# Optimization experiments

Hardware: AMD Instinct MI355X
Metric: run time of the kernel (lower is better)

## Reference

```python
import jax, jax.numpy as jnp
import numpy as np
import math

B, T, C = 2, 1400, 256
H = 16
D = C // H            # 16
FF = 1024
VOCAB = 1400
SLOTS = 256
EPS = 1e-5


def _ln(x, g, b):
    m = jnp.mean(x, axis=-1, keepdims=True)
    v = jnp.mean(jnp.square(x - m), axis=-1, keepdims=True)
    return (x - m) * jax.lax.rsqrt(v + EPS) * g + b


def setup_inputs() -> dict:
    key = jax.random.key(0)
    ks = jax.random.split(key, 24)
    s = 0.02
    inp = {
        "x": jax.random.normal(ks[0], (B, T, C), dtype=jnp.float32),
        "disease_ids": jax.random.randint(ks[1], (B, T), 0, VOCAB),
        # nn.MultiheadAttention params (torch layout: [out,in])
        "in_proj_w": jax.random.normal(ks[2], (3 * C, C)) * s,
        "in_proj_b": jnp.zeros((3 * C,), jnp.float32),
        "out_proj_w": jax.random.normal(ks[3], (C, C)) * s,
        "out_proj_b": jnp.zeros((C,), jnp.float32),
        # LayerNorms
        "ln1_g": jnp.ones((C,), jnp.float32), "ln1_b": jnp.zeros((C,), jnp.float32),
        "ln2_g": jnp.ones((C,), jnp.float32), "ln2_b": jnp.zeros((C,), jnp.float32),
        "ln3_g": jnp.ones((C,), jnp.float32), "ln3_b": jnp.zeros((C,), jnp.float32),
        # DiseaseGraphAttention
        "gq_w": jax.random.normal(ks[4], (C, C)) * s, "gq_b": jnp.zeros((C,), jnp.float32),
        "gk_w": jax.random.normal(ks[5], (C, C)) * s, "gk_b": jnp.zeros((C,), jnp.float32),
        "gv_w": jax.random.normal(ks[6], (C, C)) * s, "gv_b": jnp.zeros((C,), jnp.float32),
        "go_w": jax.random.normal(ks[7], (C, C)) * s, "go_b": jnp.zeros((C,), jnp.float32),
        "affinity": jax.random.normal(ks[8], (VOCAB, VOCAB)) * 0.01,
        # LongTermMemoryBank (only the read path affects the returned output)
        "mem_bank": jax.random.normal(ks[9], (SLOTS, C)) * 0.1,
        "read_w": jax.random.normal(ks[10], (SLOTS, C)) * s,
        "read_b": jnp.zeros((SLOTS,), jnp.float32),
        # FFN
        "ffn_w1": jax.random.normal(ks[11], (FF, C)) * s, "ffn_b1": jnp.zeros((FF,), jnp.float32),
        "ffn_w2": jax.random.normal(ks[12], (C, FF)) * s, "ffn_b2": jnp.zeros((C,), jnp.float32),
    }
    return inp


def reference(x, disease_ids, in_proj_w, in_proj_b, out_proj_w, out_proj_b,
              ln1_g, ln1_b, ln2_g, ln2_b, ln3_g, ln3_b,
              gq_w, gq_b, gk_w, gk_b, gv_w, gv_b, go_w, go_b, affinity,
              mem_bank, read_w, read_b, ffn_w1, ffn_b1, ffn_w2, ffn_b2):
    scale = 1.0 / math.sqrt(D)

    # ---- standard MHA (pre-norm, residual), dropout in eval mode ----
    h = _ln(x, ln1_g, ln1_b)
    qkv = h @ in_proj_w.T + in_proj_b                      # [B,T,3C]
    q, k, v = jnp.split(qkv, 3, axis=-1)
    q = q.reshape(B, T, H, D); k = k.reshape(B, T, H, D); v = v.reshape(B, T, H, D)
    scores = jnp.einsum('bthd,bshd->bhts', q, k) * scale   # [B,H,T,T]
    attn = jax.nn.softmax(scores, axis=-1)
    o = jnp.einsum('bhts,bshd->bthd', attn, v).reshape(B, T, C)
    x = x + (o @ out_proj_w.T + out_proj_b)

    # ---- disease-graph attention with gathered affinity bias ----
    h = _ln(x, ln2_g, ln2_b)
    q = (h @ gq_w.T + gq_b).reshape(B, T, H, D)
    k = (h @ gk_w.T + gk_b).reshape(B, T, H, D)
    v = (h @ gv_w.T + gv_b).reshape(B, T, H, D)
    aff = affinity[disease_ids]                            # [B,T,VOCAB] (VOCAB == T)
    scores = jnp.einsum('bthd,bshd->bhts', q, k) * scale + aff[:, None, :, :] * 0.1
    attn = jax.nn.softmax(scores, axis=-1)
    o = jnp.einsum('bhts,bshd->bthd', attn, v).reshape(B, T, C)
    x = x + (o @ go_w.T + go_b)

    # ---- memory-bank read (write/erase only mutate params, not the output) ----
    read_weights = jax.nn.softmax(x @ read_w.T + read_b, axis=-1)   # [B,T,SLOTS]
    x = x + jnp.einsum('bts,sc->btc', read_weights, mem_bank)

    # ---- FFN ----
    h = _ln(x, ln3_g, ln3_b)
    ff = jax.nn.gelu(h @ ffn_w1.T + ffn_b1, approximate=False) @ ffn_w2.T + ffn_b2
    return x + ff
```

## Files before the change

### kernel.cpp

```cpp
#include <hip/hip_runtime.h>
#include <hip/hip_bf16.h>
#include <math.h>

namespace {

typedef __attribute__((ext_vector_type(4))) float f32x4;
typedef __attribute__((ext_vector_type(8))) short s16x8;
typedef __attribute__((ext_vector_type(4))) short s16x4;
typedef unsigned short ushort_t;

constexpr int kB = 2, kT = 1400, kC = 256, kH = 16, kFF = 1024;
constexpr int kBT = kB * kT;
constexpr float kEps = 1e-5f;
constexpr int kSP = 5;
constexpr int kSLen = 280;
constexpr int SBLK = 288;
constexpr int KPITCH = 24;
constexpr float kQScale   = 0.25f * 1.4426950408889634f;
constexpr float kAffScale = 0.1f * 1.4426950408889634f;

__device__ __forceinline__ ushort_t f2bf(float f) {
    unsigned u = __float_as_uint(f);
    u += 0x7fffu + ((u >> 16) & 1u);
    return (ushort_t)(u >> 16);
}
__device__ __forceinline__ float bf2f(ushort_t u) {
    return __uint_as_float(((unsigned)u) << 16);
}
__device__ __forceinline__ unsigned pk2bf(float a, float b) {
    __hip_bfloat162 t = __float22bfloat162_rn(make_float2(a, b));
    union { __hip_bfloat162 h; unsigned u; } cv; cv.h = t;
    return cv.u;
}
__device__ __forceinline__ float fast_exp2(float x) {
    float r;
    asm("v_exp_f32 %0, %1" : "=v"(r) : "v"(x));
    return r;
}

__global__ __launch_bounds__(256) void convert_kernel(
        const float* __restrict__ in_proj_w, const float* __restrict__ gq_w,
        const float* __restrict__ gk_w, const float* __restrict__ gv_w,
        const float* __restrict__ out_proj_w, const float* __restrict__ go_w,
        const float* __restrict__ ffn_w1, const float* __restrict__ ffn_w2,
        const float* __restrict__ read_w, const float* __restrict__ mem_bank,
        const float* __restrict__ gq_b, const float* __restrict__ gk_b,
        const float* __restrict__ gv_b,
        ushort_t* __restrict__ wdst, float* __restrict__ gqkvb) {
    const int bid = blockIdx.x, tid = threadIdx.x;
    if (bid == 608) {
        gqkvb[tid] = gq_b[tid];
        gqkvb[256 + tid] = gk_b[tid];
        gqkvb[512 + tid] = gv_b[tid];
        return;
    }
    const int u0 = (bid * 256 + tid) * 8;
    if (u0 >= 1114112) {
        #pragma unroll
        for (int j = 0; j < 8; j++) {
            const int d = u0 - 1114112 + j;
            wdst[1114112 + d] = f2bf(mem_bank[(d & 255) * 256 + (d >> 8)]);
        }
        return;
    }
    const float* src; int off;
    if      (u0 < 196608)  { src = in_proj_w;  off = u0; }
    else if (u0 < 262144)  { src = gq_w;       off = u0 - 196608; }
    else if (u0 < 327680)  { src = gk_w;       off = u0 - 262144; }
    else if (u0 < 393216)  { src = gv_w;       off = u0 - 327680; }
    else if (u0 < 458752)  { src = out_proj_w; off = u0 - 393216; }
    else if (u0 < 524288)  { src = go_w;       off = u0 - 458752; }
    else if (u0 < 786432)  { src = ffn_w1;     off = u0 - 524288; }
    else if (u0 < 1048576) { src = ffn_w2;     off = u0 - 786432; }
    else                   { src = read_w;     off = u0 - 1048576; }
    #pragma unroll
    for (int j = 0; j < 8; j++) wdst[u0 + j] = f2bf(src[off + j]);
}

__global__ __launch_bounds__(256) void qkvln_kernel(
        const float* __restrict__ xin, const ushort_t* __restrict__ hin,
        const float* __restrict__ lng, const float* __restrict__ lnb,
        const ushort_t* __restrict__ W, const float* __restrict__ bias,
        ushort_t* __restrict__ outQ, ushort_t* __restrict__ outK,
        ushort_t* __restrict__ outV) {
    __shared__ ushort_t dsA[16 * 256];
    const int tid = threadIdx.x;
    const int lane = tid & 63, wave = tid >> 6;
    const int qi = lane & 15, g = lane >> 4;
    const int m0 = blockIdx.x * 16;

    if (xin) {
        const int r = tid >> 4, e = tid & 15;
        const float* xr = xin + (size_t)(m0 + r) * 256 + e * 16;
        const float4 v0 = *(const float4*)&xr[0];
        const float4 v1 = *(const float4*)&xr[4];
        const float4 v2 = *(const float4*)&xr[8];
        const float4 v3 = *(const float4*)&xr[12];
        float s1 = ((v0.x + v0.y) + (v0.z + v0.w)) + ((v1.x + v1.y) + (v1.z + v1.w))
                 + ((v2.x + v2.y) + (v2.z + v2.w)) + ((v3.x + v3.y) + (v3.z + v3.w));
        float s2 = ((v0.x * v0.x + v0.y * v0.y) + (v0.z * v0.z + v0.w * v0.w))
                 + ((v1.x * v1.x + v1.y * v1.y) + (v1.z * v1.z + v1.w * v1.w))
                 + ((v2.x * v2.x + v2.y * v2.y) + (v2.z * v2.z + v2.w * v2.w))
                 + ((v3.x * v3.x + v3.y * v3.y) + (v3.z * v3.z + v3.w * v3.w));
        s1 += __shfl_xor(s1, 1); s2 += __shfl_xor(s2, 1);
        s1 += __shfl_xor(s1, 2); s2 += __shfl_xor(s2, 2);
        s1 += __shfl_xor(s1, 4); s2 += __shfl_xor(s2, 4);
        s1 += __shfl_xor(s1, 8); s2 += __shfl_xor(s2, 8);
        const float mean = s1 * (1.f / 256.f);
        const float rstd = rsqrtf(s2 * (1.f / 256.f) - mean * mean + kEps);
        const int c0 = e * 16;
        const float4 ga = *(const float4*)&lng[c0];
        const float4 gb = *(const float4*)&lng[c0 + 4];
        const float4 gc = *(const float4*)&lng[c0 + 8];
        const float4 gd = *(const float4*)&lng[c0 + 12];
        const float4 ba = *(const float4*)&lnb[c0];
        const float4 bb = *(const float4*)&lnb[c0 + 4];
        const float4 bc = *(const float4*)&lnb[c0 + 8];
        const float4 bd = *(const float4*)&lnb[c0 + 12];
        union { unsigned u4[4]; s16x8 s; } p0, p1;
        p0.u4[0] = pk2bf((v0.x - mean) * rstd * ga.x + ba.x,
                         (v0.y - mean) * rstd * ga.y + ba.y);
        p0.u4[1] = pk2bf((v0.z - mean) * rstd * ga.z + ba.z,
                         (v0.w - mean) * rstd * ga.w + ba.w);
        p0.u4[2] = pk2bf((v1.x - mean) * rstd * gb.x + bb.x,
                         (v1.y - mean) * rstd * gb.y + bb.y);
        p0.u4[3] = pk2bf((v1.z - mean) * rstd * gb.z + bb.z,
                         (v1.w - mean) * rstd * gb.w + bb.w);
        p1.u4[0] = pk2bf((v2.x - mean) * rstd * gc.x + bc.x,
                         (v2.y - mean) * rstd * gc.y + bc.y);
        p1.u4[1] = pk2bf((v2.z - mean) * rstd * gc.z + bc.z,
                         (v2.w - mean) * rstd * gc.w + bc.w);
        p1.u4[2] = pk2bf((v3.x - mean) * rstd * gd.x + bd.x,
                         (v3.y - mean) * rstd * gd.y + bd.y);
        p1.u4[3] = pk2bf((v3.z - mean) * rstd * gd.z + bd.z,
                         (v3.w - mean) * rstd * gd.w + bd.w);
        const int cg0 = e * 2, cg1 = e * 2 + 1;
        *(s16x8*)&dsA[r * 256 + ((cg0 ^ (r & 7)) << 3)] = p0.s;
        *(s16x8*)&dsA[r * 256 + ((cg1 ^ (r & 7)) << 3)] = p1.s;
    } else {
        const int r = tid >> 4, e = tid & 15;
        const ushort_t* hr = hin + (size_t)(m0 + r) * 256 + e * 16;
        #pragma unroll
        for (int i = 0; i < 2; i++) {
            const s16x8 v = *(const s16x8*)&hr[i * 8];
            const int cg = e * 2 + i;
            *(s16x8*)&dsA[r * 256 + ((cg ^ (r & 7)) << 3)] = v;
        }
    }
    __syncthreads();
    f32x4 acc[12] = {};
    const int cbase = wave * 192;
    for (int kt = 0; kt < 8; ++kt) {
        const int cg = kt * 4 + g;
        const s16x8 af = *(const s16x8*)&dsA[qi * 256 + ((cg ^ (qi & 7)) << 3)];
        #pragma unroll
        for (int nn = 0; nn < 12; ++nn) {
            const int wr = cbase + nn * 16 + qi;
            const s16x8 bf = *(const s16x8*)&W[(size_t)wr * 256 + kt * 32 + g * 8];
            acc[nn] = __builtin_amdgcn_mfma_f32_16x16x32_bf16(af, bf, acc[nn], 0, 0, 0);
        }
    }
    #pragma unroll
    for (int nn = 0; nn < 12; ++nn) {
        const int col = cbase + nn * 16 + qi;
        const float bv = bias[col];
        const int hh = (col & 255) >> 4, dd = col & 15;
        #pragma unroll
        for (int r = 0; r < 4; ++r) {
            const int gm = m0 + 4 * g + r;
            const int b = (gm >= kT) ? 1 : 0;
            const int ss = gm - b * kT;
            const size_t hoff = (((size_t)(b * 16 + hh)) * kT + ss) * 16 + dd;
            const float v = acc[nn][r] + bv;
            if (col < 256)      outQ[hoff] = f2bf(v * kQScale);
            else if (col < 512) outK[hoff] = f2bf(v);
            else                outV[hoff] = f2bf(v);
        }
    }
}

__global__ __launch_bounds__(256) void ffn_kernel(
        const ushort_t* __restrict__ hin, const ushort_t* __restrict__ wF1,
        const float* __restrict__ b1, const ushort_t* __restrict__ wF2,
        const float* __restrict__ b2, const float* __restrict__ x3,
        float* __restrict__ out) {
    __shared__ ushort_t dsH[16 * 256];
    __shared__ ushort_t dsF[16 * 1024];
    const int tid = threadIdx.x;
    const int lane = tid & 63, wave = tid >> 6;
    const int qi = lane & 15, g = lane >> 4;
    const int wn = wave * 64;
    const int m0 = blockIdx.x * 16;

    {
        const int r = tid >> 4, e = tid & 15;
        const ushort_t* hr = hin + (size_t)(m0 + r) * 256 + e * 16;
        #pragma unroll
        for (int i = 0; i < 2; i++) {
            const s16x8 v = *(const s16x8*)&hr[i * 8];
            const int cg = e * 2 + i;
            *(s16x8*)&dsH[r * 256 + ((cg ^ (r & 7)) << 3)] = v;
        }
    }
    __syncthreads();
    #pragma unroll
    for (int cc = 0; cc < 4; ++cc) {
        f32x4 acc[4] = {};
        for (int kt = 0; kt < 8; ++kt) {
            const int cg = kt * 4 + g;
            const s16x8 af = *(const s16x8*)&dsH[qi * 256 + ((cg ^ (qi & 7)) << 3)];
            #pragma unroll
            for (int nn = 0; nn < 4; ++nn) {
                const int wr = cc * 256 + wn + nn * 16 + qi;
                const s16x8 bf = *(const s16x8*)&wF1[(size_t)wr * 256 + kt * 32 + g * 8];
                acc[nn] = __builtin_amdgcn_mfma_f32_16x16x32_bf16(af, bf, acc[nn], 0, 0, 0);
            }
        }
        #pragma unroll
        for (int nn = 0; nn < 4; ++nn) {
            const int col = cc * 256 + wn + nn * 16 + qi;
            const float bv = b1[col];
            #pragma unroll
            for (int r = 0; r < 4; ++r) {
                const int row = 4 * g + r;
                float v = acc[nn][r] + bv;
                v = 0.5f * v * (1.f + erff(v * 0.70710678f));
                const int cg = col >> 3, e = col & 7;
                dsF[row * 1024 + ((cg ^ (row & 7)) << 3) + e] = f2bf(v);
            }
        }
    }
    __syncthreads();
    f32x4 acc2[4] = {};
    for (int kt = 0; kt < 32; ++kt) {
        const int cg = kt * 4 + g;
        const s16x8 af = *(const s16x8*)&dsF[qi * 1024 + ((cg ^ (qi & 7)) << 3)];
        #pragma unroll
        for (int nn = 0; nn < 4; ++nn) {
            const int wr = wn + nn * 16 + qi;
            const s16x8 bf = *(const s16x8*)&wF2[(size_t)wr * 1024 + kt * 32 + g * 8];
            acc2[nn] = __builtin_amdgcn_mfma_f32_16x16x32_bf16(af, bf, acc2[nn], 0, 0, 0);
        }
    }
    #pragma unroll
    for (int nn = 0; nn < 4; ++nn) {
        const int col = wn + nn * 16 + qi;
        const float bv = b2[col];
        #pragma unroll
        for (int r = 0; r < 4; ++r) {
            const int row = 4 * g + r;
            const size_t idx = (size_t)(m0 + row) * 256 + col;
            out[idx] = acc2[nn][r] + bv + x3[idx];
        }
    }
}

__global__ __launch_bounds__(256) void gemmcomb_kernel(
        const ushort_t* __restrict__ o_part, const float* __restrict__ l_part,
        const ushort_t* __restrict__ W, const float* __restrict__ bias,
        const float* __restrict__ res,
        const float* __restrict__ lng, const float* __restrict__ lnb,
        float* __restrict__ outf, ushort_t* __restrict__ outln) {
    __shared__ ushort_t dsA[16 * 256];
    __shared__ float ws1[4][16], ws2[4][16];
    const int tid = threadIdx.x;
    const int lane = tid & 63, wave = tid >> 6;
    const int qi = lane & 15, g = lane >> 4;
    const int wn = wave * 64;
    const int m0 = blockIdx.x * 16;

    {
        const int h = tid >> 4, r = tid & 15;
        const int gm = m0 + r;
        const int b = (gm >= kT) ? 1 : 0;
        const int t = gm - b * kT;
        float f[16] = {};
        float l = 0.f;
        #pragma unroll
        for (int p = 0; p < kSP; ++p) {
            const size_t sl_ = (size_t)((b * kSP + p) * 16 + h);
            l += l_part[sl_ * kT + t];
            const s16x8 v0 = *(const s16x8*)&o_part[(sl_ * kT + t) * 16];
            const s16x8 v1 = *(const s16x8*)&o_part[(sl_ * kT + t) * 16 + 8];
            #pragma unroll
            for (int j = 0; j < 8; j++) {
                f[j]     += bf2f((ushort_t)v0[j]);
                f[8 + j] += bf2f((ushort_t)v1[j]);
            }
        }
        const float li = 1.f / l;
        union { unsigned u4[4]; s16x8 s; } p0, p1;
        p0.u4[0] = pk2bf(f[0] * li, f[1] * li);
        p0.u4[1] = pk2bf(f[2] * li, f[3] * li);
        p0.u4[2] = pk2bf(f[4] * li, f[5] * li);
        p0.u4[3] = pk2bf(f[6] * li, f[7] * li);
        p1.u4[0] = pk2bf(f[8] * li, f[9] * li);
        p1.u4[1] = pk2bf(f[10] * li, f[11] * li);
        p1.u4[2] = pk2bf(f[12] * li, f[13] * li);
        p1.u4[3] = pk2bf(f[14] * li, f[15] * li);
        const int cg0 = h * 2, cg1 = h * 2 + 1;
        *(s16x8*)&dsA[r * 256 + ((cg0 ^ (r & 7)) << 3)] = p0.s;
        *(s16x8*)&dsA[r * 256 + ((cg1 ^ (r & 7)) << 3)] = p1.s;
    }
    __syncthreads();
    f32x4 acc[4] = {};
    for (int kt = 0; kt < 8; ++kt) {
        const int cg = kt * 4 + g;
        const s16x8 af = *(const s16x8*)&dsA[qi * 256 + ((cg ^ (qi & 7)) << 3)];
        #pragma unroll
        for (int nn = 0; nn < 4; ++nn) {
            const int wr = wn + nn * 16 + qi;
            const s16x8 bf = *(const s16x8*)&W[(size_t)wr * 256 + kt * 32 + g * 8];
            acc[nn] = __builtin_amdgcn_mfma_f32_16x16x32_bf16(af, bf, acc[nn], 0, 0, 0);
        }
    }
    float v[4][4];
    float s1[4] = {0.f, 0.f, 0.f, 0.f}, s2[4] = {0.f, 0.f, 0.f, 0.f};
    #pragma unroll
    for (int nn = 0; nn < 4; ++nn) {
        #pragma unroll
        for (int r = 0; r < 4; ++r) {
            const int row = 4 * g + r, col = wn + nn * 16 + qi;
            const size_t idx = (size_t)(m0 + row) * 256 + col;
            const float t = acc[nn][r] + bias[col] + res[idx];
            outf[idx] = t;
            v[nn][r] = t;
            s1[r] += t; s2[r] += t * t;
        }
    }
    if (outln) {
        #pragma unroll
        for (int r = 0; r < 4; ++r) {
            s1[r] += __shfl_xor(s1[r], 1); s2[r] += __shfl_xor(s2[r], 1);
            s1[r] += __shfl_xor(s1[r], 2); s2[r] += __shfl_xor(s2[r], 2);
            s1[r] += __shfl_xor(s1[r], 4); s2[r] += __shfl_xor(s2[r], 4);
            s1[r] += __shfl_xor(s1[r], 8); s2[r] += __shfl_xor(s2[r], 8);
        }
        if (qi == 0) {
            #pragma unroll
            for (int r = 0; r < 4; ++r) { ws1[wave][4 * g + r] = s1[r]; ws2[wave][4 * g + r] = s2[r]; }
        }
        __syncthreads();
        #pragma unroll
        for (int r = 0; r < 4; ++r) {
            const int row = 4 * g + r;
            const float S1 = ws1[0][row] + ws1[1][row] + ws1[2][row] + ws1[3][row];
            const float S2 = ws2[0][row] + ws2[1][row] + ws2[2][row] + ws2[3][row];
            const float mean = S1 * (1.f / 256.f);
            const float rstd = rsqrtf(S2 * (1.f / 256.f) - mean * mean + kEps);
            #pragma unroll
            for (int nn = 0; nn < 4; ++nn) {
                const int col = wn + nn * 16 + qi;
                outln[(size_t)(m0 + row) * 256 + col] =
                    f2bf((v[nn][r] - mean) * rstd * lng[col] + lnb[col]);
            }
        }
    }
}

__global__ __launch_bounds__(256) void memread_kernel(
        const float* __restrict__ x2, const ushort_t* __restrict__ wRead,
        const float* __restrict__ read_b, const ushort_t* __restrict__ wMemT,
        const float* __restrict__ lng, const float* __restrict__ lnb,
        float* __restrict__ xout, ushort_t* __restrict__ outln) {
    __shared__ ushort_t dsP[16 * 256];
    __shared__ float lsum[4][16];
    __shared__ float lt[16];
    __shared__ float ws1[4][16], ws2[4][16];
    const int tid = threadIdx.x;
    const int lane = tid & 63, wave = tid >> 6;
    const int qi = lane & 15, g = lane >> 4;
    const int wn = wave * 64;
    const int m0 = blockIdx.x * 16;

    {
        const int r = tid >> 4, e = tid & 15;
        const float* xr = x2 + (size_t)(m0 + r) * 256 + e * 16;
        #pragma unroll
        for (int i = 0; i < 2; i++) {
            const float4 va = *(const float4*)&xr[i * 8];
            const float4 vb = *(const float4*)&xr[i * 8 + 4];
            union { unsigned u4[4]; s16x8 s; } pu;
            pu.u4[0] = pk2bf(va.x, va.y);
            pu.u4[1] = pk2bf(va.z, va.w);
            pu.u4[2] = pk2bf(vb.x, vb.y);
            pu.u4[3] = pk2bf(vb.z, vb.w);
            const int cg = e * 2 + i;
            *(s16x8*)&dsP[r * 256 + ((cg ^ (r & 7)) << 3)] = pu.s;
        }
    }
    __syncthreads();
    f32x4 acc[4] = {};
    for (int kt = 0; kt < 8; ++kt) {
        const int cg = kt * 4 + g;
        const s16x8 af = *(const s16x8*)&dsP[qi * 256 + ((cg ^ (qi & 7)) << 3)];
        #pragma unroll
        for (int nn = 0; nn < 4; ++nn) {
            const int wr = wn + nn * 16 + qi;
            const s16x8 bf = *(const s16x8*)&wRead[(size_t)wr * 256 + kt * 32 + g * 8];
            acc[nn] = __builtin_amdgcn_mfma_f32_16x16x32_bf16(af, bf, acc[nn], 0, 0, 0);
        }
    }
    float p[4][4];
    float rs[4] = {0.f, 0.f, 0.f, 0.f};
    #pragma unroll
    for (int nn = 0; nn < 4; ++nn) {
        const float bb = read_b[wn + nn * 16 + qi];
        #pragma unroll
        for (int r = 0; r < 4; ++r) {
            p[nn][r] = __expf(acc[nn][r] + bb);
            rs[r] += p[nn][r];
        }
    }
    #pragma unroll
    for (int r = 0; r < 4; ++r) {
        rs[r] += __shfl_xor(rs[r], 1);
        rs[r] += __shfl_xor(rs[r], 2);
        rs[r] += __shfl_xor(rs[r], 4);
        rs[r] += __shfl_xor(rs[r], 8);
    }
    __syncthreads();
    if (qi == 0) {
        #pragma unroll
        for (int r = 0; r < 4; ++r) lsum[wave][4 * g + r] = rs[r];
    }
    #pragma unroll
    for (int nn = 0; nn < 4; ++nn) {
        #pragma unroll
        for (int r = 0; r < 4; ++r) {
            const int row = 4 * g + r, col = wn + nn * 16 + qi;
            const int cg = col >> 3, e = col & 7;
            dsP[row * 256 + ((cg ^ (row & 7)) << 3) + e] = f2bf(p[nn][r]);
        }
    }
    __syncthreads();
    if (tid < 16)
        lt[tid] = 1.f / (lsum[0][tid] + lsum[1][tid] + lsum[2][tid] + lsum[3][tid]);
    __syncthreads();
    f32x4 acc2[4] = {};
    for (int kt = 0; kt < 8; ++kt) {
        const int cg = kt * 4 + g;
        const s16x8 af = *(const s16x8*)&dsP[qi * 256 + ((cg ^ (qi & 7)) << 3)];
        #pragma unroll
        for (int nn = 0; nn < 4; ++nn) {
            const int wr = wn + nn * 16 + qi;
            const s16x8 bf = *(const s16x8*)&wMemT[(size_t)wr * 256 + kt * 32 + g * 8];
            acc2[nn] = __builtin_amdgcn_mfma_f32_16x16x32_bf16(af, bf, acc2[nn], 0, 0, 0);
        }
    }
    float xo[4][4];
    float s1[4] = {0.f, 0.f, 0.f, 0.f}, s2[4] = {0.f, 0.f, 0.f, 0.f};
    #pragma unroll
    for (int nn = 0; nn < 4; ++nn) {
        #pragma unroll
        for (int r = 0; r < 4; ++r) {
            const int row = 4 * g + r;
            const size_t idx = (size_t)(m0 + row) * 256 + wn + nn * 16 + qi;
            const float t = acc2[nn][r] * lt[row] + x2[idx];
            xout[idx] = t;
            xo[nn][r] = t;
            s1[r] += t; s2[r] += t * t;
        }
    }
    #pragma unroll
    for (int r = 0; r < 4; ++r) {
        s1[r] += __shfl_xor(s1[r], 1); s2[r] += __shfl_xor(s2[r], 1);
        s1[r] += __shfl_xor(s1[r], 2); s2[r] += __shfl_xor(s2[r], 2);
        s1[r] += __shfl_xor(s1[r], 4); s2[r] += __shfl_xor(s2[r], 4);
        s1[r] += __shfl_xor(s1[r], 8); s2[r] += __shfl_xor(s2[r], 8);
    }
    if (qi == 0) {
        #pragma unroll
        for (int r = 0; r < 4; ++r) { ws1[wave][4 * g + r] = s1[r]; ws2[wave][4 * g + r] = s2[r]; }
    }
    __syncthreads();
    #pragma unroll
    for (int r = 0; r < 4; ++r) {
        const int row = 4 * g + r;
        const float S1 = ws1[0][row] + ws1[1][row] + ws1[2][row] + ws1[3][row];
        const float S2 = ws2[0][row] + ws2[1][row] + ws2[2][row] + ws2[3][row];
        const float mean = S1 * (1.f / 256.f);
        const float rstd = rsqrtf(S2 * (1.f / 256.f) - mean * mean + kEps);
        #pragma unroll
        for (int nn = 0; nn < 4; ++nn) {
            const int col = wn + nn * 16 + qi;
            outln[(size_t)(m0 + row) * 256 + col] =
                f2bf((xo[nn][r] - mean) * rstd * lng[col] + lnb[col]);
        }
    }
}

template <bool kAff>
__global__ __launch_bounds__(512) void attn_mfma_kernel(
        const ushort_t* __restrict__ q, const ushort_t* __restrict__ kbuf,
        const ushort_t* __restrict__ vbuf, ushort_t* __restrict__ o_part,
        float* __restrict__ l_part,
        const float* __restrict__ affinity, const int* __restrict__ did) {
    __shared__ ushort_t ldsK[SBLK * KPITCH];
    __shared__ ushort_t ldsV[SBLK * 16];
    const int tid  = threadIdx.x;
    const int bid  = blockIdx.x;
    const int w    = (bid & 7) * 220 + (bid >> 3);
    const int slice = w / 11;
    const int ttile = w - slice * 11;
    const int h    = slice & 15;
    const int z    = slice >> 4;
    const int b    = (z >= 5) ? 1 : 0;
    const int sp   = z - b * 5;
    const int t0   = ttile * 128;
    const int s0   = sp * kSLen;
    const int lane = tid & 63;
    const int wave = tid >> 6;
    const int g    = lane >> 4;
    const int qi   = lane & 15;

    const int tq  = t0 + wave * 16 + qi;
    const int tqc = min(tq, kT - 1);
    const ushort_t* qhb = q + (size_t)(b * 16 + h) * kT * 16;
    s16x8 qb = {0, 0, 0, 0, 0, 0, 0, 0};
    if (g < 2) qb = *(const s16x8*)&qhb[(size_t)tqc * 16 + g * 8];
    const float* ar = nullptr;
    if (kAff) ar = affinity + (size_t)did[b * kT + tqc] * kT;

    const ushort_t* kb  = kbuf + (size_t)(b * 16 + h) * kT * 16;
    const ushort_t* vbp = vbuf + (size_t)(b * 16 + h) * kT * 16;
    for (int i = tid; i < SBLK * 2; i += 512) {
        const int sl = i >> 1, hf = i & 1;
        const int sg = min(s0 + sl, kT - 1);
        *(s16x8*)&ldsK[sl * KPITCH + hf * 8] =
            *(const s16x8*)&kb[(size_t)sg * 16 + hf * 8];
        *(s16x8*)&ldsV[sl * 16 + hf * 8] =
            *(const s16x8*)&vbp[(size_t)sg * 16 + hf * 8];
    }
    __syncthreads();

    f32x4 acc = {0.f, 0.f, 0.f, 0.f};
    float lrun = 0.f;
    const unsigned vaddr = (unsigned)(size_t)(&ldsV[0]) + lane * 8;
    s16x4 va0, va1;
    asm volatile("ds_read_b64_tr_b16 %0, %2\n\t"
                 "ds_read_b64_tr_b16 %1, %2 offset:512"
                 : "=&v"(va0), "=&v"(va1) : "v"(vaddr));

    #pragma unroll
    for (int c = 0; c < SBLK / 32; ++c) {
        const int sl0 = c * 32;
        const bool tail = (c == 8);
        const s16x8 ka0 = *(const s16x8*)&ldsK[(sl0 + qi) * KPITCH + (g & 1) * 8];
        const s16x8 ka1 = *(const s16x8*)&ldsK[(sl0 + 16 + qi) * KPITCH + (g & 1) * 8];
        const f32x4 z4 = {0.f, 0.f, 0.f, 0.f};
        f32x4 d0 = __builtin_amdgcn_mfma_f32_16x16x32_bf16(ka0, qb, z4, 0, 0, 0);
        f32x4 d1 = __builtin_amdgcn_mfma_f32_16x16x32_bf16(ka1, qb, z4, 0, 0, 0);
        float sv[8];
        #pragma unroll
        for (int r = 0; r < 4; r++) { sv[r] = d0[r]; sv[4 + r] = d1[r]; }
        if (kAff) {
            if (!tail) {
                const float4 a0 = *(const float4*)&ar[s0 + sl0 + 4 * g];
                const float4 a1 = *(const float4*)&ar[s0 + sl0 + 16 + 4 * g];
                sv[0] += kAffScale * a0.x; sv[1] += kAffScale * a0.y;
                sv[2] += kAffScale * a0.z; sv[3] += kAffScale * a0.w;
                sv[4] += kAffScale * a1.x; sv[5] += kAffScale * a1.y;
                sv[6] += kAffScale * a1.z; sv[7] += kAffScale * a1.w;
            } else {
                #pragma unroll
                for (int jj = 0; jj < 8; jj++) {
                    const int s_ = s0 + sl0 + 16 * (jj >> 2) + 4 * g + (jj & 3);
                    sv[jj] += kAffScale * ar[min(s_, kT - 1)];
                }
            }
        }
        float pv[8];
        #pragma unroll
        for (int jj = 0; jj < 8; jj++) pv[jj] = fast_exp2(sv[jj]);
        if (tail && g >= 2) { pv[4] = 0.f; pv[5] = 0.f; pv[6] = 0.f; pv[7] = 0.f; }
        lrun += ((pv[0] + pv[1]) + (pv[2] + pv[3])) + ((pv[4] + pv[5]) + (pv[6] + pv[7]));
        union { unsigned u[4]; s16x8 s; } pu;
        pu.u[0] = pk2bf(pv[0], pv[1]);
        pu.u[1] = pk2bf(pv[2], pv[3]);
        pu.u[2] = pk2bf(pv[4], pv[5]);
        pu.u[3] = pk2bf(pv[6], pv[7]);
        asm volatile("s_waitcnt lgkmcnt(0)" ::: "memory");
        __builtin_amdgcn_sched_barrier(0);
        s16x8 af;
        #pragma unroll
        for (int j = 0; j < 4; j++) { af[j] = va0[j]; af[4 + j] = va1[j]; }
        acc = __builtin_amdgcn_mfma_f32_16x16x32_bf16(af, pu.s, acc, 0, 0, 0);
        if (c < SBLK / 32 - 1) {
            asm volatile("ds_read_b64_tr_b16 %0, %2\n\t"
                         "ds_read_b64_tr_b16 %1, %2 offset:512"
                         : "=&v"(va0), "=&v"(va1) : "v"(vaddr + (sl0 + 32) * 32));
        }
    }
    lrun += __shfl_xor(lrun, 16);
    lrun += __shfl_xor(lrun, 32);
    const int slice_id = (b * kSP + sp) * 16 + h;
    if (lane < 16 && tq < kT)
        l_part[(size_t)slice_id * kT + tq] = lrun;
    ushort_t* ob = o_part + (size_t)slice_id * kT * 16;
    s16x4 ov;
    #pragma unroll
    for (int r = 0; r < 4; r++) ov[r] = (short)f2bf(acc[r]);
    if (tq < kT) *(s16x4*)&ob[(size_t)tq * 16 + 4 * g] = ov;
}

}

extern "C" void kernel_launch(void* const* d_in, const int* in_sizes, int n_in,
                              void* d_out, int out_size, void* d_ws, size_t ws_size,
                              hipStream_t stream) {
    const float* x          = (const float*)d_in[0];
    const int*   did        = (const int*)d_in[1];
    const float* in_proj_w  = (const float*)d_in[2];
    const float* in_proj_b  = (const float*)d_in[3];
    const float* out_proj_w = (const float*)d_in[4];
    const float* out_proj_b = (const float*)d_in[5];
    const float* ln1_g = (const float*)d_in[6];
    const float* ln1_b = (const float*)d_in[7];
    const float* ln2_g = (const float*)d_in[8];
    const float* ln2_b = (const float*)d_in[9];
    const float* ln3_g = (const float*)d_in[10];
    const float* ln3_b = (const float*)d_in[11];
    const float* gq_w = (const float*)d_in[12];
    const float* gq_b = (const float*)d_in[13];
    const float* gk_w = (const float*)d_in[14];
    const float* gk_b = (const float*)d_in[15];
    const float* gv_w = (const float*)d_in[16];
    const float* gv_b = (const float*)d_in[17];
    const float* go_w = (const float*)d_in[18];
    const float* go_b = (const float*)d_in[19];
    const float* affinity = (const float*)d_in[20];
    const float* mem_bank = (const float*)d_in[21];
    const float* read_w   = (const float*)d_in[22];
    const float* read_b   = (const float*)d_in[23];
    const float* ffn_w1 = (const float*)d_in[24];
    const float* ffn_b1 = (const float*)d_in[25];
    const float* ffn_w2 = (const float*)d_in[26];
    const float* ffn_b2 = (const float*)d_in[27];

    char* wsb = (char*)d_ws;
    ushort_t* o_part  = (ushort_t*)(wsb + 0);
    float*    l_part  = (float*)(wsb + 7168000);
    float*    bufD    = (float*)(wsb + 13798400);
    ushort_t* bufA16  = (ushort_t*)(wsb + 16665600);
    float*    bufD2   = (float*)(wsb + 18099200);
    ushort_t* bufQ16  = (ushort_t*)(wsb + 20966400);
    ushort_t* bufK16  = (ushort_t*)(wsb + 22400000);
    ushort_t* bufV16  = (ushort_t*)(wsb + 23833600);
    ushort_t* wdst    = (ushort_t*)(wsb + 26700800);
    float*    gqkvb   = (float*)(wsb + 29191168);

    const ushort_t* wQKV1 = wdst;
    const ushort_t* wG    = wdst + 196608;
    const ushort_t* wO    = wdst + 393216;
    const ushort_t* wGO   = wdst + 458752;
    const ushort_t* wF1   = wdst + 524288;
    const ushort_t* wF2   = wdst + 786432;
    const ushort_t* wRead = wdst + 1048576;
    const ushort_t* wMemT = wdst + 1114112;

    const dim3 blk(256);
    const dim3 g_row(kBT / 16);
    const dim3 g_at(11 * kH * kB * kSP);

    convert_kernel<<<609, blk, 0, stream>>>(in_proj_w, gq_w, gk_w, gv_w, out_proj_w,
                                            go_w, ffn_w1, ffn_w2, read_w, mem_bank,
                                            gq_b, gk_b, gv_b, wdst, gqkvb);
    qkvln_kernel<<<g_row, blk, 0, stream>>>(x, nullptr, ln1_g, ln1_b,
                                            wQKV1, in_proj_b,
                                            bufQ16, bufK16, bufV16);
    attn_mfma_kernel<false><<<g_at, dim3(512), 0, stream>>>(bufQ16, bufK16, bufV16,
                                                            o_part, l_part,
                                                            nullptr, nullptr);
    gemmcomb_kernel<<<g_row, blk, 0, stream>>>(o_part, l_part, wO, out_proj_b,
                                               x, ln2_g, ln2_b, bufD2, bufA16);
    qkvln_kernel<<<g_row, blk, 0, stream>>>(nullptr, bufA16, nullptr, nullptr,
                                            wG, gqkvb,
                                            bufQ16, bufK16, bufV16);
    attn_mfma_kernel<true><<<g_at, dim3(512), 0, stream>>>(bufQ16, bufK16, bufV16,
                                                           o_part, l_part,
                                                           affinity, did);
    gemmcomb_kernel<<<g_row, blk, 0, stream>>>(o_part, l_part, wGO, go_b,
                                               bufD2, nullptr, nullptr,
                                               bufD, nullptr);
    memread_kernel<<<g_row, blk, 0, stream>>>(bufD, wRead, read_b, wMemT,
                                              ln3_g, ln3_b, bufD, bufA16);
    ffn_kernel<<<g_row, blk, 0, stream>>>(bufA16, wF1, ffn_b1, wF2, ffn_b2,
                                          bufD, (float*)d_out);
}
```

Before: 174.2 us.

## Split fused FFN into two LDS-tiled 64x64 MFMA GEMM launches

```diff
diff --git a/kernel.cpp b/kernel.cpp
--- a/kernel.cpp
+++ b/kernel.cpp
@@ -75,6 +75,75 @@
     else                   { src = read_w;     off = u0 - 1048576; }
     #pragma unroll
     for (int j = 0; j < 8; j++) wdst[u0 + j] = f2bf(src[off + j]);
+}
+
+__global__ __launch_bounds__(256) void gemm16_kernel(
+        const ushort_t* __restrict__ A, const ushort_t* __restrict__ W,
+        const float* __restrict__ bias, const float* __restrict__ res,
+        float* __restrict__ outf, ushort_t* __restrict__ outb,
+        int M, int N, int K, int ldo, int act) {
+    __shared__ ushort_t dsA[64 * 64];
+    __shared__ ushort_t dsW[64 * 64];
+    const int tid = threadIdx.x;
+    const int lane = tid & 63, wave = tid >> 6;
+    const int qi = lane & 15, g = lane >> 4;
+    const int wm = (wave >> 1) * 32, wn = (wave & 1) * 32;
+    const int m0 = blockIdx.x * 64, n0 = blockIdx.y * 64;
+
+    f32x4 acc[2][2] = {};
+    for (int kt = 0; kt < K; kt += 64) {
+        __syncthreads();
+        #pragma unroll
+        for (int j = 0; j < 2; ++j) {
+            const int u = tid + j * 256;
+            const int row = u >> 3, c = u & 7;
+            const int cs = c ^ (row & 7);
+            const int gmA = min(m0 + row, M - 1);
+            *(s16x8*)&dsA[row * 64 + cs * 8] =
+                *(const s16x8*)&A[(size_t)gmA * K + kt + c * 8];
+            *(s16x8*)&dsW[row * 64 + cs * 8] =
+                *(const s16x8*)&W[(size_t)(n0 + row) * K + kt + c * 8];
+        }
+        __syncthreads();
+        #pragma unroll
+        for (int kk = 0; kk < 2; ++kk) {
+            s16x8 af[2], bf[2];
+            #pragma unroll
+            for (int f = 0; f < 2; ++f) {
+                const int r = wm + f * 16 + qi;
+                af[f] = *(const s16x8*)&dsA[r * 64 + (((kk * 4 + g) ^ (r & 7)) * 8)];
+            }
+            #pragma unroll
+            for (int nn = 0; nn < 2; ++nn) {
+                const int r = wn + nn * 16 + qi;
+                bf[nn] = *(const s16x8*)&dsW[r * 64 + (((kk * 4 + g) ^ (r & 7)) * 8)];
+            }
+            #pragma unroll
+            for (int f = 0; f < 2; ++f)
+                #pragma unroll
+                for (int nn = 0; nn < 2; ++nn)
+                    acc[f][nn] = __builtin_amdgcn_mfma_f32_16x16x32_bf16(
+                        af[f], bf[nn], acc[f][nn], 0, 0, 0);
+        }
+    }
+    #pragma unroll
+    for (int f = 0; f < 2; ++f) {
+        #pragma unroll
+        for (int r = 0; r < 4; ++r) {
+            const int gm = m0 + wm + f * 16 + g * 4 + r;
+            if (gm >= M) continue;
+            #pragma unroll
+            for (int nn = 0; nn < 2; ++nn) {
+                const int gn = n0 + wn + nn * 16 + qi;
+                float v = acc[f][nn][r];
+                if (bias) v += bias[gn];
+                if (act == 1) v = 0.5f * v * (1.f + erff(v * 0.70710678f));
+                if (res) v += res[(size_t)gm * ldo + gn];
+                if (outf) outf[(size_t)gm * ldo + gn] = v;
+                if (outb) outb[(size_t)gm * ldo + gn] = f2bf(v);
+            }
+        }
+    }
 }
 
 __global__ __launch_bounds__(256) void qkvln_kernel(
@@ -179,82 +248,6 @@
     }
 }
 
-__global__ __launch_bounds__(256) void ffn_kernel(
-        const ushort_t* __restrict__ hin, const ushort_t* __restrict__ wF1,
-        const float* __restrict__ b1, const ushort_t* __restrict__ wF2,
-        const float* __restrict__ b2, const float* __restrict__ x3,
-        float* __restrict__ out) {
-    __shared__ ushort_t dsH[16 * 256];
-    __shared__ ushort_t dsF[16 * 1024];
-    const int tid = threadIdx.x;
-    const int lane = tid & 63, wave = tid >> 6;
-    const int qi = lane & 15, g = lane >> 4;
-    const int wn = wave * 64;
-    const int m0 = blockIdx.x * 16;
-
-    {
-        const int r = tid >> 4, e = tid & 15;
-        const ushort_t* hr = hin + (size_t)(m0 + r) * 256 + e * 16;
-        #pragma unroll
-        for (int i = 0; i < 2; i++) {
-            const s16x8 v = *(const s16x8*)&hr[i * 8];
-            const int cg = e * 2 + i;
-            *(s16x8*)&dsH[r * 256 + ((cg ^ (r & 7)) << 3)] = v;
-        }
-    }
-    __syncthreads();
-    #pragma unroll
-    for (int cc = 0; cc < 4; ++cc) {
-        f32x4 acc[4] = {};
-        for (int kt = 0; kt < 8; ++kt) {
-            const int cg = kt * 4 + g;
-            const s16x8 af = *(const s16x8*)&dsH[qi * 256 + ((cg ^ (qi & 7)) << 3)];
-            #pragma unroll
-            for (int nn = 0; nn < 4; ++nn) {
-                const int wr = cc * 256 + wn + nn * 16 + qi;
-                const s16x8 bf = *(const s16x8*)&wF1[(size_t)wr * 256 + kt * 32 + g * 8];
-                acc[nn] = __builtin_amdgcn_mfma_f32_16x16x32_bf16(af, bf, acc[nn], 0, 0, 0);
-            }
-        }
-        #pragma unroll
-        for (int nn = 0; nn < 4; ++nn) {
-            const int col = cc * 256 + wn + nn * 16 + qi;
-            const float bv = b1[col];
-            #pragma unroll
-            for (int r = 0; r < 4; ++r) {
-                const int row = 4 * g + r;
-                float v = acc[nn][r] + bv;
-                v = 0.5f * v * (1.f + erff(v * 0.70710678f));
-                const int cg = col >> 3, e = col & 7;
-                dsF[row * 1024 + ((cg ^ (row & 7)) << 3) + e] = f2bf(v);
-            }
-        }
-    }
-    __syncthreads();
-    f32x4 acc2[4] = {};
-    for (int kt = 0; kt < 32; ++kt) {
-        const int cg = kt * 4 + g;
-        const s16x8 af = *(const s16x8*)&dsF[qi * 1024 + ((cg ^ (qi & 7)) << 3)];
-        #pragma unroll
-        for (int nn = 0; nn < 4; ++nn) {
-            const int wr = wn + nn * 16 + qi;
-            const s16x8 bf = *(const s16x8*)&wF2[(size_t)wr * 1024 + kt * 32 + g * 8];
-            acc2[nn] = __builtin_amdgcn_mfma_f32_16x16x32_bf16(af, bf, acc2[nn], 0, 0, 0);
-        }
-    }
-    #pragma unroll
-    for (int nn = 0; nn < 4; ++nn) {
-        const int col = wn + nn * 16 + qi;
-        const float bv = b2[col];
-        #pragma unroll
-        for (int r = 0; r < 4; ++r) {
-            const int row = 4 * g + r;
-            const size_t idx = (size_t)(m0 + row) * 256 + col;
-            out[idx] = acc2[nn][r] + bv + x3[idx];
-        }
-    }
-}
-
 __global__ __launch_bounds__(256) void gemmcomb_kernel(
         const ushort_t* __restrict__ o_part, const float* __restrict__ l_part,
         const ushort_t* __restrict__ W, const float* __restrict__ bias,
@@ -641,6 +634,7 @@
     char* wsb = (char*)d_ws;
     ushort_t* o_part  = (ushort_t*)(wsb + 0);
     float*    l_part  = (float*)(wsb + 7168000);
+    ushort_t* ff116   = (ushort_t*)(wsb + 8064000);
     float*    bufD    = (float*)(wsb + 13798400);
     ushort_t* bufA16  = (ushort_t*)(wsb + 16665600);
     float*    bufD2   = (float*)(wsb + 18099200);
@@ -660,6 +654,8 @@
     const ushort_t* wMemT = wdst + 1114112;
 
     const dim3 blk(256);
+    const int MT = (kBT + 63) / 64;
+    const dim3 g_c(MT, 4), g_ff(MT, 16);
     const dim3 g_row(kBT / 16);
     const dim3 g_at(11 * kH * kB * kSP);
 
@@ -685,6 +681,8 @@
                                                bufD, nullptr);
     memread_kernel<<<g_row, blk, 0, stream>>>(bufD, wRead, read_b, wMemT,
                                               ln3_g, ln3_b, bufD, bufA16);
-    ffn_kernel<<<g_row, blk, 0, stream>>>(bufA16, wF1, ffn_b1, wF2, ffn_b2,
-                                          bufD, (float*)d_out);
-}
+    gemm16_kernel<<<g_ff, blk, 0, stream>>>(bufA16, wF1, ffn_b1, nullptr,
+                                            nullptr, ff116, kBT, kFF, kC, kFF, 1);
+    gemm16_kernel<<<g_c, blk, 0, stream>>>(ff116, wF2, ffn_b2, bufD,
+                                           (float*)d_out, nullptr, kBT, kC, kFF, kC, 0);
+}
```

After: 155.1 us. 1.12x faster.
